# Kernel tuning notes

Measured on AMD Instinct MI355X. Metric: run time of the kernel, lower is better.

Reference implementation:

```python
import jax, jax.numpy as jnp
import numpy as np

B, D, H, O, E = 65536, 128, 256, 8, 8  # batch, input_dim, hidden_dim, output_dim, n_phases


def setup_inputs() -> dict:
    key = jax.random.key(0)
    ks = jax.random.split(key, 6)
    scale = 0.05
    x = jax.random.normal(ks[0], (B, D), dtype=jnp.float32)
    phases = jax.random.randint(ks[1], (B,), 0, E, dtype=jnp.int32)
    Ws = jax.random.normal(ks[2], (D, H), dtype=jnp.float32) * scale  # shared Linear weight (transposed)
    bs = jnp.zeros((H,), dtype=jnp.float32)
    W1 = jax.random.normal(ks[3], (E, H, H), dtype=jnp.float32) * scale  # per-head first Linear
    b1 = jnp.zeros((E, H), dtype=jnp.float32)
    W2 = jax.random.normal(ks[4], (E, H, O), dtype=jnp.float32) * scale  # per-head second Linear
    b2 = jnp.zeros((E, O), dtype=jnp.float32)
    return {"x": x, "phases": phases, "Ws": Ws, "bs": bs,
            "W1": W1, "b1": b1, "W2": W2, "b2": b2}


def reference(x, phases, Ws, bs, W1, b1, W2, b2):
    # shared trunk: Linear + ReLU
    h = jax.nn.relu(x @ Ws + bs)                                # [B, H]
    # run every head on every sample (dense grouped GEMM), then gather the
    # per-sample routed head. NOTE: no activation between the two head Linears,
    # matching nn.Sequential(Linear, Linear) in the source.
    h1 = jnp.einsum('bh,ehk->ebk', h, W1) + b1[:, None, :]      # [E, B, H]
    y = jnp.einsum('ebk,eko->ebo', h1, W2) + b2[:, None, :]     # [E, B, O]
    q = y[phases, jnp.arange(x.shape[0])]                       # [B, O] routed select
    return q
```

## Files before the change

kernel.cpp:

```cpp
#include <hip/hip_runtime.h>
#include <hip/hip_bf16.h>
#include <cstdint>


using bf16x8 = __attribute__((ext_vector_type(8))) __bf16;
using f32x4  = __attribute__((ext_vector_type(4))) float;

__device__ __forceinline__ unsigned short bf16b(float f) {
    __bf16 h = (__bf16)f;
    return __builtin_bit_cast(unsigned short, h);
}
__device__ __forceinline__ unsigned pack2(float a, float b) {
    return (unsigned)bf16b(a) | ((unsigned)bf16b(b) << 16);
}

__global__ void prep_kernel(const float* __restrict__ Ws,
                            const float* __restrict__ b1,
                            const float* __restrict__ W1,
                            const float* __restrict__ W2,
                            const float* __restrict__ b2,
                            uint4* __restrict__ wsP,
                            unsigned short* __restrict__ wfP,
                            float* __restrict__ bfuse) {
    const int bid = blockIdx.x, tid = threadIdx.x;
    if (bid < 256) {
        __shared__ float w2sT[8][256];
        const int e = bid >> 5, mc = bid & 31;
        const float* W2e = W2 + (size_t)e * 2048;
        float4 v0 = ((const float4*)W2e)[tid];
        float4 v1 = ((const float4*)W2e)[256 + tid];
        const int mloc = tid >> 5, kg = tid & 31;
        const int m = mc * 8 + mloc;
        const float* w1row = W1 + ((size_t)e * 256 + m) * 256;
        float w1v[8];
        #pragma unroll
        for (int i = 0; i < 8; ++i) w1v[i] = w1row[kg + i * 32];
        {
            int f4 = tid, k = f4 >> 1, o4 = (f4 & 1) * 4;
            w2sT[o4 + 0][k] = v0.x; w2sT[o4 + 1][k] = v0.y;
            w2sT[o4 + 2][k] = v0.z; w2sT[o4 + 3][k] = v0.w;
            f4 = 256 + tid; k = f4 >> 1; o4 = (f4 & 1) * 4;
            w2sT[o4 + 0][k] = v1.x; w2sT[o4 + 1][k] = v1.y;
            w2sT[o4 + 2][k] = v1.z; w2sT[o4 + 3][k] = v1.w;
        }
        __syncthreads();
        float acc[8] = {0,0,0,0,0,0,0,0};
        #pragma unroll
        for (int i = 0; i < 8; ++i) {
            int k = kg + i * 32;
            #pragma unroll
            for (int o = 0; o < 8; ++o) acc[o] += w1v[i] * w2sT[o][k];
        }
        #pragma unroll
        for (int o = 0; o < 8; ++o) {
            acc[o] += __shfl_xor(acc[o], 1);
            acc[o] += __shfl_xor(acc[o], 2);
            acc[o] += __shfl_xor(acc[o], 4);
            acc[o] += __shfl_xor(acc[o], 8);
            acc[o] += __shfl_xor(acc[o], 16);
        }
        if (kg == 0) {
            const int kgf  = m >> 5;
            const int lhif = (m >> 3) & 3;
            const int j    = m & 7;
            #pragma unroll
            for (int o = 0; o < 8; ++o) {
                int c = e * 8 + o;
                int lanef = lhif * 16 + (c & 15);
                int F = (kgf * 4 + (c >> 4)) * 64 + lanef;
                wfP[(size_t)F * 8 + j] = bf16b(acc[o]);
            }
        }
    } else if (bid < 272) {
        const int b2i = bid - 256;
        const int kg = b2i >> 2, hi = b2i & 3;
        const int wv = tid >> 6, lane = tid & 63;
        const int l15 = lane & 15, lhi = lane >> 4;
        const int n  = wv * 64 + hi * 16 + l15;
        const int k0 = kg * 32 + lhi * 8;
        float w[8];
        #pragma unroll
        for (int j = 0; j < 8; ++j)
            w[j] = Ws[(size_t)(k0 + j) * 256 + n];
        uint4 u;
        u.x = pack2(w[0], w[1]); u.y = pack2(w[2], w[3]);
        u.z = pack2(w[4], w[5]); u.w = pack2(w[6], w[7]);
        wsP[((kg * 4 + hi) * 4 + wv) * 64 + lane] = u;
    } else {
        const int e = tid >> 5, l = tid & 31;
        float acc[8] = {0,0,0,0,0,0,0,0};
        #pragma unroll
        for (int i = 0; i < 8; ++i) {
            int k = l * 8 + i;
            float a = b1[e * 256 + k];
            const float* w2r = W2 + ((size_t)(e * 256 + k)) * 8;
            #pragma unroll
            for (int o = 0; o < 8; ++o) acc[o] += a * w2r[o];
        }
        #pragma unroll
        for (int o = 0; o < 8; ++o) {
            acc[o] += __shfl_xor(acc[o], 1);
            acc[o] += __shfl_xor(acc[o], 2);
            acc[o] += __shfl_xor(acc[o], 4);
            acc[o] += __shfl_xor(acc[o], 8);
            acc[o] += __shfl_xor(acc[o], 16);
        }
        if (l == 0) {
            #pragma unroll
            for (int o = 0; o < 8; ++o)
                bfuse[e * 8 + o] = acc[o] + b2[e * 8 + o];
        }
    }
}

__global__ __launch_bounds__(256) void fused_kernel(
    const float* __restrict__ x,
    const int* __restrict__ phases,
    const float* __restrict__ bs,
    const uint4* __restrict__ wsP,
    const uint4* __restrict__ wfP,
    const float* __restrict__ bfuse,
    float* __restrict__ out) {
    __shared__ __align__(16) char lds[8192 + 16384];
    char* xs = lds;
    char* hs = lds + 8192;

    const int tid = threadIdx.x;
    const int lane = tid & 63;
    const int wv = tid >> 6;
    const int l15 = lane & 15;
    const int lhi = lane >> 4;
    const int row0 = blockIdx.x * 32;

    const float4* xg = (const float4*)x;

    float4 a0[2], d0[2];
    #pragma unroll
    for (int it = 0; it < 2; ++it) {
        int c = it * 256 + tid;
        int row = c >> 4, col8 = c & 15;
        int gi = (row0 + row) * 32 + col8 * 2;
        a0[it] = xg[gi]; d0[it] = xg[gi + 1];
    }

    bf16x8 wsA[4][4];
    #pragma unroll
    for (int hi = 0; hi < 4; ++hi)
        #pragma unroll
        for (int kg = 0; kg < 4; ++kg)
            wsA[hi][kg] = __builtin_bit_cast(bf16x8,
                wsP[((kg * 4 + hi) * 4 + wv) * 64 + lane]);

    f32x4 bsv[4];
    #pragma unroll
    for (int hi = 0; hi < 4; ++hi)
        bsv[hi] = *(const f32x4*)(bs + wv * 64 + hi * 16 + lhi * 4);
    const float bfv = bfuse[wv * 16 + l15];
    const int myE = wv * 2 + (l15 >> 3);
    const int co  = l15 & 7;
    int ev[8];
    #pragma unroll
    for (int mi = 0; mi < 2; ++mi)
        #pragma unroll
        for (int r = 0; r < 4; ++r)
            ev[mi * 4 + r] = phases[row0 + mi * 16 + lhi * 4 + r];

    #pragma unroll
    for (int it = 0; it < 2; ++it) {
        int c = it * 256 + tid;
        int row = c >> 4, col8 = c & 15;
        unsigned addr = (unsigned)(row * 256 + col8 * 16);
        addr ^= (unsigned)((row & 7) << 4);
        uint4 u;
        u.x = pack2(a0[it].x, a0[it].y); u.y = pack2(a0[it].z, a0[it].w);
        u.z = pack2(d0[it].x, d0[it].y); u.w = pack2(d0[it].z, d0[it].w);
        *(uint4*)(xs + addr) = u;
    }
    __syncthreads();

    f32x4 acc1[4][2];
    #pragma unroll
    for (int hi = 0; hi < 4; ++hi)
        #pragma unroll
        for (int bi = 0; bi < 2; ++bi)
            acc1[hi][bi] = (f32x4){0.f, 0.f, 0.f, 0.f};
    #pragma unroll
    for (int kg = 0; kg < 4; ++kg) {
        bf16x8 xb[2];
        #pragma unroll
        for (int bi = 0; bi < 2; ++bi) {
            int b = bi * 16 + l15;
            unsigned addr = (unsigned)(b * 256 + (kg * 32 + lhi * 8) * 2);
            addr ^= (unsigned)((b & 7) << 4);
            xb[bi] = *(const bf16x8*)(xs + addr);
        }
        __builtin_amdgcn_s_setprio(1);
        #pragma unroll
        for (int hi = 0; hi < 4; ++hi)
            #pragma unroll
            for (int bi = 0; bi < 2; ++bi)
                acc1[hi][bi] = __builtin_amdgcn_mfma_f32_16x16x32_bf16(
                    wsA[hi][kg], xb[bi], acc1[hi][bi], 0, 0, 0);
        __builtin_amdgcn_s_setprio(0);
    }

    bf16x8 wfB[8];
    #pragma unroll
    for (int kg = 0; kg < 8; ++kg)
        wfB[kg] = __builtin_bit_cast(bf16x8, wfP[(kg * 4 + wv) * 64 + lane]);

    #pragma unroll
    for (int hi = 0; hi < 4; ++hi)
        #pragma unroll
        for (int bi = 0; bi < 2; ++bi) {
            float v0 = acc1[hi][bi][0] + bsv[hi][0]; v0 = v0 > 0.f ? v0 : 0.f;
            float v1 = acc1[hi][bi][1] + bsv[hi][1]; v1 = v1 > 0.f ? v1 : 0.f;
            float v2 = acc1[hi][bi][2] + bsv[hi][2]; v2 = v2 > 0.f ? v2 : 0.f;
            float v3 = acc1[hi][bi][3] + bsv[hi][3]; v3 = v3 > 0.f ? v3 : 0.f;
            uint2 u; u.x = pack2(v0, v1); u.y = pack2(v2, v3);
            int b = bi * 16 + l15;
            int n0 = wv * 64 + hi * 16 + lhi * 4;
            unsigned addr = (unsigned)(b * 512 + n0 * 2);
            addr ^= (unsigned)((b & 7) << 4);
            *(uint2*)(hs + addr) = u;
        }
    __syncthreads();

    f32x4 acc2[2];
    #pragma unroll
    for (int mi = 0; mi < 2; ++mi)
        acc2[mi] = (f32x4){bfv, bfv, bfv, bfv};
    #pragma unroll
    for (int kg = 0; kg < 8; ++kg) {
        bf16x8 ha[2];
        #pragma unroll
        for (int mi = 0; mi < 2; ++mi) {
            int b = mi * 16 + l15;
            unsigned addr = (unsigned)(b * 512 + (kg * 32 + lhi * 8) * 2);
            addr ^= (unsigned)((b & 7) << 4);
            ha[mi] = *(const bf16x8*)(hs + addr);
        }
        __builtin_amdgcn_s_setprio(1);
        #pragma unroll
        for (int mi = 0; mi < 2; ++mi)
            acc2[mi] = __builtin_amdgcn_mfma_f32_16x16x32_bf16(
                ha[mi], wfB[kg], acc2[mi], 0, 0, 0);
        __builtin_amdgcn_s_setprio(0);
    }

    #pragma unroll
    for (int mi = 0; mi < 2; ++mi)
        #pragma unroll
        for (int r = 0; r < 4; ++r) {
            int b = mi * 16 + lhi * 4 + r;
            if (ev[mi * 4 + r] == myE)
                out[(size_t)(row0 + b) * 8 + co] = acc2[mi][r];
        }
}

extern "C" void kernel_launch(void* const* d_in, const int* in_sizes, int n_in,
                              void* d_out, int out_size, void* d_ws, size_t ws_size,
                              hipStream_t stream) {
    const float* x      = (const float*)d_in[0];
    const int*   phases = (const int*)d_in[1];
    const float* Ws     = (const float*)d_in[2];
    const float* bs     = (const float*)d_in[3];
    const float* W1     = (const float*)d_in[4];
    const float* b1     = (const float*)d_in[5];
    const float* W2     = (const float*)d_in[6];
    const float* b2     = (const float*)d_in[7];
    float* out = (float*)d_out;

    uint4*          wsP   = (uint4*)d_ws;
    unsigned short* wfP   = (unsigned short*)((char*)d_ws + 65536);
    float*          bfuse = (float*)((char*)d_ws + 98304);

    prep_kernel<<<273, 256, 0, stream>>>(Ws, b1, W1, W2, b2,
                                         wsP, wfP, bfuse);
    fused_kernel<<<2048, 256, 0, stream>>>(
        x, phases, bs, wsP, (const uint4*)wfP, bfuse, out);
}
```

Baseline: 23.33 us.

## Process two row tiles per block and prefetch the next x tile

The grid is halved so each block handles two 32-row tiles. The shared-trunk and fused-head weight fragments are loaded into registers once and reused for both tiles, which halves weight reloads. The second tile's x rows are loaded from global memory and written to LDS while the first tile's second GEMM is still computing. The cost is more register pressure and fewer blocks available to hide latency across the GPU.

```diff
diff --git a/kernel.cpp b/kernel.cpp
--- a/kernel.cpp
+++ b/kernel.cpp
@@ -130,17 +130,19 @@
     const int wv = tid >> 6;
     const int l15 = lane & 15;
     const int lhi = lane >> 4;
-    const int row0 = blockIdx.x * 32;
 
     const float4* xg = (const float4*)x;
 
     float4 a0[2], d0[2];
-    #pragma unroll
-    for (int it = 0; it < 2; ++it) {
-        int c = it * 256 + tid;
-        int row = c >> 4, col8 = c & 15;
-        int gi = (row0 + row) * 32 + col8 * 2;
-        a0[it] = xg[gi]; d0[it] = xg[gi + 1];
+    {
+        int row0 = blockIdx.x * 32;
+        #pragma unroll
+        for (int it = 0; it < 2; ++it) {
+            int c = it * 256 + tid;
+            int row = c >> 4, col8 = c & 15;
+            int gi = (row0 + row) * 32 + col8 * 2;
+            a0[it] = xg[gi]; d0[it] = xg[gi + 1];
+        }
     }
 
     bf16x8 wsA[4][4];
@@ -150,6 +152,10 @@
         for (int kg = 0; kg < 4; ++kg)
             wsA[hi][kg] = __builtin_bit_cast(bf16x8,
                 wsP[((kg * 4 + hi) * 4 + wv) * 64 + lane]);
+    bf16x8 wfB[8];
+    #pragma unroll
+    for (int kg = 0; kg < 8; ++kg)
+        wfB[kg] = __builtin_bit_cast(bf16x8, wfP[(kg * 4 + wv) * 64 + lane]);
 
     f32x4 bsv[4];
     #pragma unroll
@@ -158,12 +164,6 @@
     const float bfv = bfuse[wv * 16 + l15];
     const int myE = wv * 2 + (l15 >> 3);
     const int co  = l15 & 7;
-    int ev[8];
-    #pragma unroll
-    for (int mi = 0; mi < 2; ++mi)
-        #pragma unroll
-        for (int r = 0; r < 4; ++r)
-            ev[mi * 4 + r] = phases[row0 + mi * 16 + lhi * 4 + r];
 
     #pragma unroll
     for (int it = 0; it < 2; ++it) {
@@ -176,86 +176,116 @@
         u.z = pack2(d0[it].x, d0[it].y); u.w = pack2(d0[it].z, d0[it].w);
         *(uint4*)(xs + addr) = u;
     }
-    __syncthreads();
-
-    f32x4 acc1[4][2];
-    #pragma unroll
-    for (int hi = 0; hi < 4; ++hi)
-        #pragma unroll
-        for (int bi = 0; bi < 2; ++bi)
-            acc1[hi][bi] = (f32x4){0.f, 0.f, 0.f, 0.f};
-    #pragma unroll
-    for (int kg = 0; kg < 4; ++kg) {
-        bf16x8 xb[2];
-        #pragma unroll
-        for (int bi = 0; bi < 2; ++bi) {
-            int b = bi * 16 + l15;
-            unsigned addr = (unsigned)(b * 256 + (kg * 32 + lhi * 8) * 2);
-            addr ^= (unsigned)((b & 7) << 4);
-            xb[bi] = *(const bf16x8*)(xs + addr);
-        }
-        __builtin_amdgcn_s_setprio(1);
+
+    #pragma unroll
+    for (int t = 0; t < 2; ++t) {
+        const int row0 = (blockIdx.x + t * 1024) * 32;
+        __syncthreads();
+
+        f32x4 acc1[4][2];
         #pragma unroll
         for (int hi = 0; hi < 4; ++hi)
             #pragma unroll
             for (int bi = 0; bi < 2; ++bi)
-                acc1[hi][bi] = __builtin_amdgcn_mfma_f32_16x16x32_bf16(
-                    wsA[hi][kg], xb[bi], acc1[hi][bi], 0, 0, 0);
-        __builtin_amdgcn_s_setprio(0);
+                acc1[hi][bi] = (f32x4){0.f, 0.f, 0.f, 0.f};
+        #pragma unroll
+        for (int kg = 0; kg < 4; ++kg) {
+            bf16x8 xb[2];
+            #pragma unroll
+            for (int bi = 0; bi < 2; ++bi) {
+                int b = bi * 16 + l15;
+                unsigned addr = (unsigned)(b * 256 + (kg * 32 + lhi * 8) * 2);
+                addr ^= (unsigned)((b & 7) << 4);
+                xb[bi] = *(const bf16x8*)(xs + addr);
+            }
+            __builtin_amdgcn_s_setprio(1);
+            #pragma unroll
+            for (int hi = 0; hi < 4; ++hi)
+                #pragma unroll
+                for (int bi = 0; bi < 2; ++bi)
+                    acc1[hi][bi] = __builtin_amdgcn_mfma_f32_16x16x32_bf16(
+                        wsA[hi][kg], xb[bi], acc1[hi][bi], 0, 0, 0);
+            __builtin_amdgcn_s_setprio(0);
+        }
+
+        int ev[8];
+        #pragma unroll
+        for (int mi = 0; mi < 2; ++mi)
+            #pragma unroll
+            for (int r = 0; r < 4; ++r)
+                ev[mi * 4 + r] = phases[row0 + mi * 16 + lhi * 4 + r];
+
+        #pragma unroll
+        for (int hi = 0; hi < 4; ++hi)
+            #pragma unroll
+            for (int bi = 0; bi < 2; ++bi) {
+                float v0 = acc1[hi][bi][0] + bsv[hi][0]; v0 = v0 > 0.f ? v0 : 0.f;
+                float v1 = acc1[hi][bi][1] + bsv[hi][1]; v1 = v1 > 0.f ? v1 : 0.f;
+                float v2 = acc1[hi][bi][2] + bsv[hi][2]; v2 = v2 > 0.f ? v2 : 0.f;
+                float v3 = acc1[hi][bi][3] + bsv[hi][3]; v3 = v3 > 0.f ? v3 : 0.f;
+                uint2 u; u.x = pack2(v0, v1); u.y = pack2(v2, v3);
+                int b = bi * 16 + l15;
+                int n0 = wv * 64 + hi * 16 + lhi * 4;
+                unsigned addr = (unsigned)(b * 512 + n0 * 2);
+                addr ^= (unsigned)((b & 7) << 4);
+                *(uint2*)(hs + addr) = u;
+            }
+        __syncthreads();
+
+        if (t == 0) {
+            float4 a1[2], d1[2];
+            int nrow0 = (blockIdx.x + 1024) * 32;
+            #pragma unroll
+            for (int it = 0; it < 2; ++it) {
+                int c = it * 256 + tid;
+                int row = c >> 4, col8 = c & 15;
+                int gi = (nrow0 + row) * 32 + col8 * 2;
+                a1[it] = xg[gi]; d1[it] = xg[gi + 1];
+            }
+            #pragma unroll
+            for (int it = 0; it < 2; ++it) {
+                int c = it * 256 + tid;
+                int row = c >> 4, col8 = c & 15;
+                unsigned addr = (unsigned)(row * 256 + col8 * 16);
+                addr ^= (unsigned)((row & 7) << 4);
+                uint4 u;
+                u.x = pack2(a1[it].x, a1[it].y); u.y = pack2(a1[it].z, a1[it].w);
+                u.z = pack2(d1[it].x, d1[it].y); u.w = pack2(d1[it].z, d1[it].w);
+                *(uint4*)(xs + addr) = u;
+            }
+        }
+
+        f32x4 acc2[2];
+        #pragma unroll
+        for (int mi = 0; mi < 2; ++mi)
+            acc2[mi] = (f32x4){bfv, bfv, bfv, bfv};
+        #pragma unroll
+        for (int kg = 0; kg < 8; ++kg) {
+            bf16x8 ha[2];
+            #pragma unroll
+            for (int mi = 0; mi < 2; ++mi) {
+                int b = mi * 16 + l15;
+                unsigned addr = (unsigned)(b * 512 + (kg * 32 + lhi * 8) * 2);
+                addr ^= (unsigned)((b & 7) << 4);
+                ha[mi] = *(const bf16x8*)(hs + addr);
+            }
+            __builtin_amdgcn_s_setprio(1);
+            #pragma unroll
+            for (int mi = 0; mi < 2; ++mi)
+                acc2[mi] = __builtin_amdgcn_mfma_f32_16x16x32_bf16(
+                    ha[mi], wfB[kg], acc2[mi], 0, 0, 0);
+            __builtin_amdgcn_s_setprio(0);
+        }
+
+        #pragma unroll
+        for (int mi = 0; mi < 2; ++mi)
+            #pragma unroll
+            for (int r = 0; r < 4; ++r) {
+                int b = mi * 16 + lhi * 4 + r;
+                if (ev[mi * 4 + r] == myE)
+                    out[(size_t)(row0 + b) * 8 + co] = acc2[mi][r];
+            }
     }
-
-    bf16x8 wfB[8];
-    #pragma unroll
-    for (int kg = 0; kg < 8; ++kg)
-        wfB[kg] = __builtin_bit_cast(bf16x8, wfP[(kg * 4 + wv) * 64 + lane]);
-
-    #pragma unroll
-    for (int hi = 0; hi < 4; ++hi)
-        #pragma unroll
-        for (int bi = 0; bi < 2; ++bi) {
-            float v0 = acc1[hi][bi][0] + bsv[hi][0]; v0 = v0 > 0.f ? v0 : 0.f;
-            float v1 = acc1[hi][bi][1] + bsv[hi][1]; v1 = v1 > 0.f ? v1 : 0.f;
-            float v2 = acc1[hi][bi][2] + bsv[hi][2]; v2 = v2 > 0.f ? v2 : 0.f;
-            float v3 = acc1[hi][bi][3] + bsv[hi][3]; v3 = v3 > 0.f ? v3 : 0.f;
-            uint2 u; u.x = pack2(v0, v1); u.y = pack2(v2, v3);
-            int b = bi * 16 + l15;
-            int n0 = wv * 64 + hi * 16 + lhi * 4;
-            unsigned addr = (unsigned)(b * 512 + n0 * 2);
-            addr ^= (unsigned)((b & 7) << 4);
-            *(uint2*)(hs + addr) = u;
-        }
-    __syncthreads();
-
-    f32x4 acc2[2];
-    #pragma unroll
-    for (int mi = 0; mi < 2; ++mi)
-        acc2[mi] = (f32x4){bfv, bfv, bfv, bfv};
-    #pragma unroll
-    for (int kg = 0; kg < 8; ++kg) {
-        bf16x8 ha[2];
-        #pragma unroll
-        for (int mi = 0; mi < 2; ++mi) {
-            int b = mi * 16 + l15;
-            unsigned addr = (unsigned)(b * 512 + (kg * 32 + lhi * 8) * 2);
-            addr ^= (unsigned)((b & 7) << 4);
-            ha[mi] = *(const bf16x8*)(hs + addr);
-        }
-        __builtin_amdgcn_s_setprio(1);
-        #pragma unroll
-        for (int mi = 0; mi < 2; ++mi)
-            acc2[mi] = __builtin_amdgcn_mfma_f32_16x16x32_bf16(
-                ha[mi], wfB[kg], acc2[mi], 0, 0, 0);
-        __builtin_amdgcn_s_setprio(0);
-    }
-
-    #pragma unroll
-    for (int mi = 0; mi < 2; ++mi)
-        #pragma unroll
-        for (int r = 0; r < 4; ++r) {
-            int b = mi * 16 + lhi * 4 + r;
-            if (ev[mi * 4 + r] == myE)
-                out[(size_t)(row0 + b) * 8 + co] = acc2[mi][r];
-        }
 }
 
 extern "C" void kernel_launch(void* const* d_in, const int* in_sizes, int n_in,
@@ -277,6 +307,6 @@
 
     prep_kernel<<<273, 256, 0, stream>>>(Ws, b1, W1, W2, b2,
                                          wsP, wfP, bfuse);
-    fused_kernel<<<2048, 256, 0, stream>>>(
+    fused_kernel<<<1024, 256, 0, stream>>>(
         x, phases, bs, wsP, (const uint4*)wfP, bfuse, out);
 }
```

Measured after the change: 23.57 us. Within noise of the previous version (+1.0%).
